# Kernel tuning notes

Measured on AMD Instinct MI355X. Metric: run time of the kernel, lower is better.

Reference implementation:

```python
import jax, jax.numpy as jnp
import numpy as np

B_TRUE, S, HEADS, DIM_HEAD, DIM, N = 2, 2, 8, 64, 512, 1024
BS = B_TRUE * S            # effective batch = (b s)
DIM_INNER = HEADS * DIM_HEAD
ALL_HEADS = S * HEADS
EPS = 1e-5


def setup_inputs() -> dict:
    key = jax.random.key(0)
    ks = jax.random.split(key, 8)
    inv = 0.02
    x = jax.random.normal(ks[0], (BS, N, DIM), dtype=jnp.float32)
    mask = jax.random.randint(ks[1], (BS, N), 0, 2).astype(bool)
    gamma = jnp.ones((DIM,), dtype=jnp.float32)
    w_qkv = jax.random.normal(ks[2], (3 * DIM_INNER, DIM), dtype=jnp.float32) * inv
    w_gates = jax.random.normal(ks[3], (HEADS, DIM), dtype=jnp.float32) * inv
    b_gates = jnp.zeros((HEADS,), dtype=jnp.float32)
    w_pre = jax.random.normal(ks[4], (ALL_HEADS, ALL_HEADS), dtype=jnp.float32) * 0.25
    w_post = jax.random.normal(ks[5], (ALL_HEADS, ALL_HEADS), dtype=jnp.float32) * 0.25
    w_out = jax.random.normal(ks[6], (DIM, DIM_INNER), dtype=jnp.float32) * inv
    return {"x": x, "mask": mask, "gamma": gamma, "w_qkv": w_qkv,
            "w_gates": w_gates, "b_gates": b_gates, "w_pre": w_pre,
            "w_post": w_post, "w_out": w_out}


def _rmsnorm(x, gamma):
    # einn.Norm('b... [d]', mean=False, bias=False): RMSNorm over last dim
    var = jnp.mean(jnp.square(x), axis=-1, keepdims=True)
    return x * jax.lax.rsqrt(var + EPS) * gamma


def reference(x, mask, gamma, w_qkv, w_gates, b_gates, w_pre, w_post, w_out):
    bs, n, dim = x.shape
    b = bs // S
    x = _rmsnorm(x, gamma)

    # QKV: 'b n (qkv h d) -> qkv b h n d'
    qkv = jnp.einsum('bnd,ed->bne', x, w_qkv)
    qkv = qkv.reshape(bs, n, 3, HEADS, DIM_HEAD).transpose(2, 0, 3, 1, 4)
    q, k, v = qkv[0], qkv[1], qkv[2]
    q = q * (DIM_HEAD ** 0.5)  # NOTE: source MULTIPLIES by sqrt(dim_head)

    sim = jnp.einsum('bhid,bhjd->bhij', q, k)  # [bs, h, n, n]
    mask_value = -jnp.finfo(sim.dtype).max

    # pre talking-heads: 1x1 conv across (s h) channels
    sim = sim.reshape(b, ALL_HEADS, n, n)
    sim = jnp.einsum('oi,binm->bonm', w_pre, sim).reshape(bs, HEADS, n, n)

    # padding mask over keys j
    sim = jnp.where(mask[:, None, None, :], sim, mask_value)

    # causal mask
    causal = jnp.triu(jnp.ones((n, n), dtype=bool), 1)
    sim = jnp.where(causal, mask_value, sim)

    attn = jax.nn.softmax(sim, axis=-1)
    post_softmax_attn = attn

    # post talking-heads
    attn = attn.reshape(b, ALL_HEADS, n, n)
    attn = jnp.einsum('oi,binm->bonm', w_post, attn).reshape(bs, HEADS, n, n)

    out = jnp.einsum('bhij,bhjd->bhid', attn, v)  # [bs, h, n, d]

    # sigmoid gates from normed x: 'b n h -> b h n 1'
    gates = jax.nn.sigmoid(jnp.einsum('bnd,hd->bnh', x, w_gates) + b_gates)
    out = out * gates.transpose(0, 2, 1)[..., None]

    # 'b h n d -> b n (h d)' then Linear(dim_inner, dim, bias=False)
    out = out.transpose(0, 2, 1, 3).reshape(bs, n, DIM_INNER)
    out = jnp.einsum('bne,de->bnd', out, w_out)
    return (out, post_softmax_attn)
```

## Files before the change

kernel.cpp:

```cpp
#include <hip/hip_runtime.h>
#include <cfloat>
#include <math.h>

#define B2   2
#define BS4  4
#define NH   8
#define DH   64
#define DIM  512
#define NSEQ 1024
#define AH   16

typedef __attribute__((ext_vector_type(8))) short short8;
typedef __attribute__((ext_vector_type(4))) float floatx4;
typedef __attribute__((ext_vector_type(2))) float float2v;

__device__ inline unsigned short f2bf(float x) {
    unsigned int u = __float_as_uint(x);
    unsigned int r = (u + 0x7fffu + ((u >> 16) & 1u)) >> 16;
    return (unsigned short)r;
}
__device__ inline float bf2f(unsigned short h) {
    return __uint_as_float(((unsigned int)h) << 16);
}
__device__ inline void split2(float x, unsigned short& h, unsigned short& l) {
    h = f2bf(x);
    l = f2bf(x - bf2f(h));
}
__device__ inline int il_addr(int k) { return ((k >> 3) << 4) + (k & 7); }

__device__ inline float2v pk_fma(float2v a, float2v b, float2v c) {
#if __has_builtin(__builtin_elementwise_fma)
    return __builtin_elementwise_fma(a, b, c);
#else
    float2v r;
    r[0] = fmaf(a[0], b[0], c[0]);
    r[1] = fmaf(a[1], b[1], c[1]);
    return r;
#endif
}

template<int MT, int NT_, bool SPLIT, bool IL>
__device__ inline void mfma_nt_core(
    const unsigned short* __restrict__ Ah, const unsigned short* __restrict__ Al,
    const unsigned short* __restrict__ Bh, const unsigned short* __restrict__ Bl,
    int K, int lda, int ldb, int arow, int bcol, floatx4 acc[MT][NT_])
{
    int lane = threadIdx.x & 63;
    int lr = lane & 15, lq = lane >> 4;
    for (int k0 = 0; k0 < K; k0 += 32) {
        const int ka = IL ? (k0 + lq * 8) * 2 : (k0 + lq * 8);
        short8 ah[MT], al[MT], bh[NT_], bl[NT_];
        #pragma unroll
        for (int mi = 0; mi < MT; ++mi) {
            size_t off = (size_t)(arow + mi * 16 + lr) * lda + ka;
            ah[mi] = *(const short8*)(Ah + off);
            if (SPLIT) al[mi] = *(const short8*)(Al + off);
        }
        #pragma unroll
        for (int ni = 0; ni < NT_; ++ni) {
            size_t off = (size_t)(bcol + ni * 16 + lr) * ldb + ka;
            bh[ni] = *(const short8*)(Bh + off);
            if (SPLIT) bl[ni] = *(const short8*)(Bl + off);
        }
        #pragma unroll
        for (int mi = 0; mi < MT; ++mi)
            #pragma unroll
            for (int ni = 0; ni < NT_; ++ni) {
                acc[mi][ni] = __builtin_amdgcn_mfma_f32_16x16x32_bf16(ah[mi], bh[ni], acc[mi][ni], 0, 0, 0);
                if (SPLIT) {
                    acc[mi][ni] = __builtin_amdgcn_mfma_f32_16x16x32_bf16(ah[mi], bl[ni], acc[mi][ni], 0, 0, 0);
                    acc[mi][ni] = __builtin_amdgcn_mfma_f32_16x16x32_bf16(al[mi], bh[ni], acc[mi][ni], 0, 0, 0);
                }
            }
    }
}

__global__ __launch_bounds__(256) void k_rmsnorm_gates(
    const float* __restrict__ x, const float* __restrict__ gamma,
    const float* __restrict__ wg, const float* __restrict__ bg,
    unsigned short* __restrict__ xn_il, float* __restrict__ gates)
{
    int r = blockIdx.x;
    int tid = threadIdx.x;
    const float* xr = x + (size_t)r * DIM;
    float v0 = xr[tid];
    float v1 = xr[tid + 256];
    float ss = v0 * v0 + v1 * v1;
    #pragma unroll
    for (int off = 32; off > 0; off >>= 1) ss += __shfl_down(ss, off, 64);
    __shared__ float sc[4];
    __shared__ float scw[NH][4];
    if ((tid & 63) == 0) sc[tid >> 6] = ss;
    __syncthreads();
    float tot = sc[0] + sc[1] + sc[2] + sc[3];
    float rs = rsqrtf(tot * (1.0f / DIM) + 1e-5f);
    float n0 = v0 * rs * gamma[tid];
    float n1 = v1 * rs * gamma[tid + 256];
    size_t rb = (size_t)r * (2 * DIM);
    unsigned short hh, ll;
    split2(n0, hh, ll);
    int a0 = il_addr(tid);
    xn_il[rb + a0] = hh; xn_il[rb + a0 + 8] = ll;
    split2(n1, hh, ll);
    int a1 = il_addr(tid + 256);
    xn_il[rb + a1] = hh; xn_il[rb + a1 + 8] = ll;
    #pragma unroll
    for (int h = 0; h < NH; ++h) {
        float p = n0 * wg[h * DIM + tid] + n1 * wg[h * DIM + tid + 256];
        #pragma unroll
        for (int off = 32; off > 0; off >>= 1) p += __shfl_down(p, off, 64);
        if ((tid & 63) == 0) scw[h][tid >> 6] = p;
    }
    __syncthreads();
    if (tid < NH) {
        float g = scw[tid][0] + scw[tid][1] + scw[tid][2] + scw[tid][3] + bg[tid];
        gates[(size_t)r * NH + tid] = 1.0f / (1.0f + __expf(-g));
    }
}

#define NQKV (3 * DIM * NH * DH)
#define NOUT (DIM * NH * DH)
__global__ __launch_bounds__(256) void k_cvt(
    const float* __restrict__ wqkv, const float* __restrict__ wout,
    unsigned short* __restrict__ wq_il, unsigned short* __restrict__ wout_b)
{
    for (int i = blockIdx.x * 256 + threadIdx.x; i < NQKV + NOUT; i += gridDim.x * 256) {
        if (i < NQKV) {
            unsigned short hh, ll;
            split2(wqkv[i], hh, ll);
            int e = i >> 9, k = i & 511;
            size_t a = (size_t)e * (2 * DIM) + il_addr(k);
            wq_il[a] = hh; wq_il[a + 8] = ll;
        } else {
            wout_b[i - NQKV] = f2bf(wout[i - NQKV]);
        }
    }
}

__global__ __launch_bounds__(64) void k_qkv_mfma(
    const unsigned short* __restrict__ xn_il, const unsigned short* __restrict__ wq_il,
    unsigned short* __restrict__ q_il, unsigned short* __restrict__ k_il,
    unsigned short* __restrict__ vT_b)
{
    __shared__ unsigned short vs[64][68];
    int bx = blockIdx.x;
    int am = blockIdx.y * 64;
    int bn = bx * 64;
    floatx4 acc[4][4];
    #pragma unroll
    for (int mi = 0; mi < 4; ++mi)
        #pragma unroll
        for (int ni = 0; ni < 4; ++ni) acc[mi][ni] = (floatx4){0.f, 0.f, 0.f, 0.f};
    mfma_nt_core<4, 4, true, true>(xn_il, xn_il + 8, wq_il, wq_il + 8,
                                   DIM, 2 * DIM, 2 * DIM, am, bn, acc);
    int tid = threadIdx.x;
    int lane = tid & 63, lr = lane & 15, lq = lane >> 4;

    if (bx < 16) {
        const bool isq = (bx < 8);
        unsigned short* dst = isq ? q_il : k_il;
        const float scale = isq ? 8.0f : 1.0f;
        #pragma unroll
        for (int mi = 0; mi < 4; ++mi)
            #pragma unroll
            for (int ni = 0; ni < 4; ++ni)
                #pragma unroll
                for (int r = 0; r < 4; ++r) {
                    int row = am + mi * 16 + lq * 4 + r;
                    int col = bn + ni * 16 + lr;
                    int bs = row >> 10, npos = row & 1023;
                    int h = (col >> 6) & 7, d = col & 63;
                    size_t base = (((size_t)(bs * 8 + h)) * NSEQ + npos) * (2 * DH) + il_addr(d);
                    unsigned short hh, ll;
                    split2(acc[mi][ni][r] * scale, hh, ll);
                    dst[base] = hh; dst[base + 8] = ll;
                }
    } else {
        const int h = bx - 16;
        const int bs = (blockIdx.y * 64) >> 10;
        const int bh = bs * 8 + h;
        const int npos_base = (blockIdx.y * 64) & 1023;
        #pragma unroll
        for (int mi = 0; mi < 4; ++mi)
            #pragma unroll
            for (int ni = 0; ni < 4; ++ni)
                #pragma unroll
                for (int r = 0; r < 4; ++r) {
                    int nl  = mi * 16 + lq * 4 + r;
                    int dl2 = ni * 16 + lr;
                    vs[dl2][nl] = f2bf(acc[mi][ni][r]);
                }
        __syncthreads();
        #pragma unroll
        for (int it = 0; it < 8; ++it) {
            int d = it * 8 + (tid >> 3);
            int c8 = (tid & 7) * 8;
            unsigned short* dst = vT_b + ((size_t)bh * DH + d) * NSEQ + npos_base + c8;
            *(ulonglong2*)dst = *(ulonglong2*)&vs[d][c8];
        }
    }
}

__global__ __launch_bounds__(64) void k_qk_mfma(
    const unsigned short* __restrict__ q_il, const unsigned short* __restrict__ k_il,
    float* __restrict__ sim_ws)
{
    __shared__ float cs[64][68];
    int am0 = blockIdx.y * 64;
    int bn0 = blockIdx.x * 64;
    if (bn0 > am0 + 63) return;
    int bh = blockIdx.z;
    int b_true = bh >> 4;
    int c = ((bh >> 3) & 1) * 8 + (bh & 7);
    const unsigned short* A = q_il + (size_t)bh * NSEQ * (2 * DH);
    const unsigned short* B = k_il + (size_t)bh * NSEQ * (2 * DH);
    floatx4 acc[4][4];
    #pragma unroll
    for (int mi = 0; mi < 4; ++mi)
        #pragma unroll
        for (int ni = 0; ni < 4; ++ni) acc[mi][ni] = (floatx4){0.f, 0.f, 0.f, 0.f};
    mfma_nt_core<4, 4, true, true>(A, A + 8, B, B + 8, DH, 2 * DH, 2 * DH, am0, bn0, acc);

    int tid = threadIdx.x;
    int lane = tid & 63, lr = lane & 15, lq = lane >> 4;
    #pragma unroll
    for (int mi = 0; mi < 4; ++mi)
        #pragma unroll
        for (int ni = 0; ni < 4; ++ni)
            #pragma unroll
            for (int r = 0; r < 4; ++r) {
                int lrow = mi * 16 + lq * 4 + r;
                int lcol = ni * 16 + lr;
                cs[lrow][lcol] = acc[mi][ni][r];
            }
    __syncthreads();
    int trow = tid >> 4;
    int tcol = (tid & 15) * 4;
    #pragma unroll
    for (int it = 0; it < 16; ++it) {
        int row = it * 4 + trow;
        float4 v4 = *(float4*)&cs[row][tcol];
        size_t gaddr = ((size_t)(b_true * NSEQ + am0 + row) * 16 + c) * NSEQ + bn0 + tcol;
        *(float4*)(sim_ws + gaddr) = v4;
    }
}

__global__ __launch_bounds__(256) void k_talk(
    float* __restrict__ sim_ws, const int* __restrict__ mask,
    const float* __restrict__ wpre, const float* __restrict__ wpost,
    float* __restrict__ probs_out)
{
    const int i = blockIdx.x;
    const int b = blockIdx.y;
    const int tid = threadIdx.x;
    const int wid = tid >> 6, lane = tid & 63;
    const int j0 = tid << 2;
    const size_t cstride = (size_t)NSEQ * NSEQ;
    float* simrow = sim_ws + (size_t)(b * NSEQ + i) * (16 * NSEQ);

    const int4 mi0 = *(const int4*)(mask + (size_t)(b * 2 + 0) * NSEQ + j0);
    const int4 mi1 = *(const int4*)(mask + (size_t)(b * 2 + 1) * NSEQ + j0);
    bool mb[2][4];
    mb[0][0] = (mi0.x != 0) && (j0 + 0 <= i);
    mb[0][1] = (mi0.y != 0) && (j0 + 1 <= i);
    mb[0][2] = (mi0.z != 0) && (j0 + 2 <= i);
    mb[0][3] = (mi0.w != 0) && (j0 + 3 <= i);
    mb[1][0] = (mi1.x != 0) && (j0 + 0 <= i);
    mb[1][1] = (mi1.y != 0) && (j0 + 1 <= i);
    mb[1][2] = (mi1.z != 0) && (j0 + 2 <= i);
    mb[1][3] = (mi1.w != 0) && (j0 + 3 <= i);

    float2v val[16][2];
    #pragma unroll
    for (int o = 0; o < 16; ++o) {
        val[o][0] = (float2v){0.f, 0.f};
        val[o][1] = (float2v){0.f, 0.f};
    }
    #pragma unroll
    for (int c = 0; c < 16; ++c) {
        float4 r = *(const float4*)(simrow + c * NSEQ + j0);
        float2v r01 = (float2v){r.x, r.y};
        float2v r23 = (float2v){r.z, r.w};
        #pragma unroll
        for (int o = 0; o < 16; ++o) {
            float w = wpre[o * 16 + c];
            float2v wv = (float2v){w, w};
            val[o][0] = pk_fma(wv, r01, val[o][0]);
            val[o][1] = pk_fma(wv, r23, val[o][1]);
        }
    }
    #pragma unroll
    for (int o = 0; o < 16; ++o) {
        const int s = o >> 3;
        if (!mb[s][0]) val[o][0][0] = -FLT_MAX;
        if (!mb[s][1]) val[o][0][1] = -FLT_MAX;
        if (!mb[s][2]) val[o][1][0] = -FLT_MAX;
        if (!mb[s][3]) val[o][1][1] = -FLT_MAX;
    }

    __shared__ float red[16][4];
    __shared__ float finmx[16];
    __shared__ float fininv[16];

    #pragma unroll
    for (int o = 0; o < 16; ++o) {
        float m = fmaxf(fmaxf(val[o][0][0], val[o][0][1]), fmaxf(val[o][1][0], val[o][1][1]));
        #pragma unroll
        for (int off = 32; off > 0; off >>= 1) m = fmaxf(m, __shfl_xor(m, off, 64));
        if (lane == 0) red[o][wid] = m;
    }
    __syncthreads();
    if (tid < 16)
        finmx[tid] = fmaxf(fmaxf(red[tid][0], red[tid][1]), fmaxf(red[tid][2], red[tid][3]));
    __syncthreads();

    #pragma unroll
    for (int o = 0; o < 16; ++o) {
        float mx = finmx[o];
        float e0 = __expf(val[o][0][0] - mx);
        float e1 = __expf(val[o][0][1] - mx);
        float e2 = __expf(val[o][1][0] - mx);
        float e3 = __expf(val[o][1][1] - mx);
        val[o][0][0] = e0; val[o][0][1] = e1;
        val[o][1][0] = e2; val[o][1][1] = e3;
        float s = (e0 + e1) + (e2 + e3);
        #pragma unroll
        for (int off = 32; off > 0; off >>= 1) s += __shfl_xor(s, off, 64);
        if (lane == 0) red[o][wid] = s;
    }
    __syncthreads();
    if (tid < 16)
        fininv[tid] = 1.0f / (red[tid][0] + red[tid][1] + red[tid][2] + red[tid][3]);
    __syncthreads();

    #pragma unroll
    for (int o = 0; o < 16; ++o) {
        float inv = fininv[o];
        float2v invv = (float2v){inv, inv};
        val[o][0] *= invv;
        val[o][1] *= invv;
        floatx4 st = {val[o][0][0], val[o][0][1], val[o][1][0], val[o][1][1]};
        __builtin_nontemporal_store(st,
            (floatx4*)(probs_out + (size_t)(b * 16 + o) * cstride + (size_t)i * NSEQ + j0));
    }

    unsigned short* a2row = (unsigned short*)simrow;
    #pragma unroll
    for (int o = 0; o < 16; ++o) {
        float2v a01 = (float2v){0.f, 0.f};
        float2v a23 = (float2v){0.f, 0.f};
        #pragma unroll
        for (int c = 0; c < 16; ++c) {
            float w = wpost[o * 16 + c];
            float2v wv = (float2v){w, w};
            a01 = pk_fma(wv, val[c][0], a01);
            a23 = pk_fma(wv, val[c][1], a23);
        }
        unsigned long long pk = (unsigned long long)f2bf(a01[0])
                              | ((unsigned long long)f2bf(a01[1]) << 16)
                              | ((unsigned long long)f2bf(a23[0]) << 32)
                              | ((unsigned long long)f2bf(a23[1]) << 48);
        *(unsigned long long*)(a2row + o * NSEQ + j0) = pk;
    }
}

__global__ __launch_bounds__(64) void k_av_mfma(
    const unsigned short* __restrict__ attn2_il, const unsigned short* __restrict__ vT_b,
    const float* __restrict__ gates, unsigned short* __restrict__ gated_b)
{
    int bh = blockIdx.y;
    int bs = bh >> 3, h = bh & 7;
    int b_true = bh >> 4;
    int c = ((bh >> 3) & 1) * 8 + (bh & 7);
    int am = blockIdx.x * 64;
    const unsigned short* Ah = attn2_il + (size_t)b_true * NSEQ * 32768 + (size_t)c * NSEQ;
    const unsigned short* Bh = vT_b + (size_t)bh * DH * NSEQ;
    floatx4 acc[4][4];
    #pragma unroll
    for (int mi = 0; mi < 4; ++mi)
        #pragma unroll
        for (int ni = 0; ni < 4; ++ni) acc[mi][ni] = (floatx4){0.f, 0.f, 0.f, 0.f};
    mfma_nt_core<4, 4, false, false>(Ah, nullptr, Bh, nullptr, NSEQ, 32768, NSEQ, am, 0, acc);
    int lane = threadIdx.x & 63, lr = lane & 15, lq = lane >> 4;
    #pragma unroll
    for (int mi = 0; mi < 4; ++mi)
        #pragma unroll
        for (int ni = 0; ni < 4; ++ni)
            #pragma unroll
            for (int r = 0; r < 4; ++r) {
                int i = am + mi * 16 + lq * 4 + r;
                int d = ni * 16 + lr;
                float g = gates[((size_t)bs * NSEQ + i) * NH + h];
                gated_b[((size_t)bs * NSEQ + i) * DIM + h * DH + d] = f2bf(acc[mi][ni][r] * g);
            }
}

__global__ __launch_bounds__(64) void k_out_mfma(
    const unsigned short* __restrict__ gated_b, const unsigned short* __restrict__ wout_b,
    float* __restrict__ out)
{
    int am = blockIdx.y * 64;
    int bn = blockIdx.x * 64;
    floatx4 acc[4][4];
    #pragma unroll
    for (int mi = 0; mi < 4; ++mi)
        #pragma unroll
        for (int ni = 0; ni < 4; ++ni) acc[mi][ni] = (floatx4){0.f, 0.f, 0.f, 0.f};
    mfma_nt_core<4, 4, false, false>(gated_b, nullptr, wout_b, nullptr, DIM, DIM, DIM, am, bn, acc);
    int lane = threadIdx.x & 63, lr = lane & 15, lq = lane >> 4;
    #pragma unroll
    for (int mi = 0; mi < 4; ++mi)
        #pragma unroll
        for (int ni = 0; ni < 4; ++ni)
            #pragma unroll
            for (int r = 0; r < 4; ++r) {
                int row = am + mi * 16 + lq * 4 + r;
                int col = bn + ni * 16 + lr;
                out[(size_t)row * DIM + col] = acc[mi][ni][r];
            }
}

extern "C" void kernel_launch(void* const* d_in, const int* in_sizes, int n_in,
                              void* d_out, int out_size, void* d_ws, size_t ws_size,
                              hipStream_t stream)
{
    (void)in_sizes; (void)n_in; (void)out_size; (void)ws_size;

    const float* x     = (const float*)d_in[0];
    const int*   mask  = (const int*)  d_in[1];
    const float* gamma = (const float*)d_in[2];
    const float* wqkv  = (const float*)d_in[3];
    const float* wg    = (const float*)d_in[4];
    const float* bg    = (const float*)d_in[5];
    const float* wpre  = (const float*)d_in[6];
    const float* wpost = (const float*)d_in[7];
    const float* wout  = (const float*)d_in[8];

    float* out       = (float*)d_out;
    float* probs_out = out + (size_t)BS4 * NSEQ * DIM;

    char* ws = (char*)d_ws;
    unsigned short* xn_il   = (unsigned short*)(ws);
    unsigned short* wq_il   = (unsigned short*)(ws + 8388608);
    unsigned short* wout_b  = (unsigned short*)(ws + 11534336);
    float*          gates   = (float*)         (ws + 12058624);
    unsigned short* q_il    = (unsigned short*)(ws + 12189696);
    unsigned short* k_il    = (unsigned short*)(ws + 20578304);
    unsigned short* vT_b    = (unsigned short*)(ws + 28966912);
    unsigned short* gated_b = (unsigned short*)(ws + 33161216);
    float*          sim_ws  = (float*)         (ws + 37355520);

    k_rmsnorm_gates<<<dim3(BS4 * NSEQ), dim3(256), 0, stream>>>(x, gamma, wg, bg, xn_il, gates);
    k_cvt<<<dim3(1024), dim3(256), 0, stream>>>(wqkv, wout, wq_il, wout_b);
    k_qkv_mfma<<<dim3(24, 64), dim3(64), 0, stream>>>(xn_il, wq_il, q_il, k_il, vT_b);
    k_qk_mfma<<<dim3(16, 16, 32), dim3(64), 0, stream>>>(q_il, k_il, sim_ws);
    k_talk<<<dim3(NSEQ, B2), dim3(256), 0, stream>>>(sim_ws, mask, wpre, wpost, probs_out);
    k_av_mfma<<<dim3(16, 32), dim3(64), 0, stream>>>((unsigned short*)sim_ws, vT_b, gates, gated_b);
    k_out_mfma<<<dim3(8, 64), dim3(64), 0, stream>>>(gated_b, wout_b, out);
}
```

Measured before the change: 373.2 us.

## Fuse prep kernels, trim softmax barriers, split-K across two waves in AV/out GEMMs

Merges the RMSNorm/gates kernel and the weight-conversion kernel into one launch, using extra blocks for the conversion. In the talking-heads softmax, each thread now reduces the per-wave partials itself, which removes two barriers and two shared-memory stages. The AV and output-projection GEMMs use two waves per block, each taking half of K, with the partials combined through shared memory. This raises parallelism in the low-occupancy GEMMs at the cost of extra LDS traffic and a barrier.

```diff
diff --git a/kernel.cpp b/kernel.cpp
--- a/kernel.cpp
+++ b/kernel.cpp
@@ -75,13 +75,34 @@
     }
 }
 
-__global__ __launch_bounds__(256) void k_rmsnorm_gates(
+#define NQKV (3 * DIM * NH * DH)
+#define NOUT (DIM * NH * DH)
+__global__ __launch_bounds__(256) void k_prep(
     const float* __restrict__ x, const float* __restrict__ gamma,
     const float* __restrict__ wg, const float* __restrict__ bg,
-    unsigned short* __restrict__ xn_il, float* __restrict__ gates)
-{
+    const float* __restrict__ wqkv, const float* __restrict__ wout,
+    unsigned short* __restrict__ xn_il, float* __restrict__ gates,
+    unsigned short* __restrict__ wq_il, unsigned short* __restrict__ wout_b)
+{
+    int tid = threadIdx.x;
+    if (blockIdx.x >= BS4 * NSEQ) {
+        int base = (blockIdx.x - BS4 * NSEQ) * 2048;
+        #pragma unroll
+        for (int e = 0; e < 8; ++e) {
+            int i = base + e * 256 + tid;
+            if (i < NQKV) {
+                unsigned short hh, ll;
+                split2(wqkv[i], hh, ll);
+                int row = i >> 9, k = i & 511;
+                size_t a = (size_t)row * (2 * DIM) + il_addr(k);
+                wq_il[a] = hh; wq_il[a + 8] = ll;
+            } else {
+                wout_b[i - NQKV] = f2bf(wout[i - NQKV]);
+            }
+        }
+        return;
+    }
     int r = blockIdx.x;
-    int tid = threadIdx.x;
     const float* xr = x + (size_t)r * DIM;
     float v0 = xr[tid];
     float v1 = xr[tid + 256];
@@ -115,25 +136,6 @@
     if (tid < NH) {
         float g = scw[tid][0] + scw[tid][1] + scw[tid][2] + scw[tid][3] + bg[tid];
         gates[(size_t)r * NH + tid] = 1.0f / (1.0f + __expf(-g));
-    }
-}
-
-#define NQKV (3 * DIM * NH * DH)
-#define NOUT (DIM * NH * DH)
-__global__ __launch_bounds__(256) void k_cvt(
-    const float* __restrict__ wqkv, const float* __restrict__ wout,
-    unsigned short* __restrict__ wq_il, unsigned short* __restrict__ wout_b)
-{
-    for (int i = blockIdx.x * 256 + threadIdx.x; i < NQKV + NOUT; i += gridDim.x * 256) {
-        if (i < NQKV) {
-            unsigned short hh, ll;
-            split2(wqkv[i], hh, ll);
-            int e = i >> 9, k = i & 511;
-            size_t a = (size_t)e * (2 * DIM) + il_addr(k);
-            wq_il[a] = hh; wq_il[a + 8] = ll;
-        } else {
-            wout_b[i - NQKV] = f2bf(wout[i - NQKV]);
-        }
     }
 }
 
@@ -298,25 +300,21 @@
         if (!mb[s][3]) val[o][1][1] = -FLT_MAX;
     }
 
-    __shared__ float red[16][4];
-    __shared__ float finmx[16];
-    __shared__ float fininv[16];
+    __shared__ float red_m[16][4];
+    __shared__ float red_s[16][4];
 
     #pragma unroll
     for (int o = 0; o < 16; ++o) {
         float m = fmaxf(fmaxf(val[o][0][0], val[o][0][1]), fmaxf(val[o][1][0], val[o][1][1]));
         #pragma unroll
         for (int off = 32; off > 0; off >>= 1) m = fmaxf(m, __shfl_xor(m, off, 64));
-        if (lane == 0) red[o][wid] = m;
-    }
-    __syncthreads();
-    if (tid < 16)
-        finmx[tid] = fmaxf(fmaxf(red[tid][0], red[tid][1]), fmaxf(red[tid][2], red[tid][3]));
-    __syncthreads();
-
-    #pragma unroll
-    for (int o = 0; o < 16; ++o) {
-        float mx = finmx[o];
+        if (lane == 0) red_m[o][wid] = m;
+    }
+    __syncthreads();
+
+    #pragma unroll
+    for (int o = 0; o < 16; ++o) {
+        float mx = fmaxf(fmaxf(red_m[o][0], red_m[o][1]), fmaxf(red_m[o][2], red_m[o][3]));
         float e0 = __expf(val[o][0][0] - mx);
         float e1 = __expf(val[o][0][1] - mx);
         float e2 = __expf(val[o][1][0] - mx);
@@ -326,16 +324,13 @@
         float s = (e0 + e1) + (e2 + e3);
         #pragma unroll
         for (int off = 32; off > 0; off >>= 1) s += __shfl_xor(s, off, 64);
-        if (lane == 0) red[o][wid] = s;
-    }
-    __syncthreads();
-    if (tid < 16)
-        fininv[tid] = 1.0f / (red[tid][0] + red[tid][1] + red[tid][2] + red[tid][3]);
-    __syncthreads();
-
-    #pragma unroll
-    for (int o = 0; o < 16; ++o) {
-        float inv = fininv[o];
+        if (lane == 0) red_s[o][wid] = s;
+    }
+    __syncthreads();
+
+    #pragma unroll
+    for (int o = 0; o < 16; ++o) {
+        float inv = 1.0f / ((red_s[o][0] + red_s[o][1]) + (red_s[o][2] + red_s[o][3]));
         float2v invv = (float2v){inv, inv};
         val[o][0] *= invv;
         val[o][1] *= invv;
@@ -364,60 +359,91 @@
     }
 }
 
-__global__ __launch_bounds__(64) void k_av_mfma(
+__global__ __launch_bounds__(128) void k_av_mfma(
     const unsigned short* __restrict__ attn2_il, const unsigned short* __restrict__ vT_b,
     const float* __restrict__ gates, unsigned short* __restrict__ gated_b)
 {
+    __shared__ float cls[64][68];
     int bh = blockIdx.y;
     int bs = bh >> 3, h = bh & 7;
     int b_true = bh >> 4;
     int c = ((bh >> 3) & 1) * 8 + (bh & 7);
     int am = blockIdx.x * 64;
-    const unsigned short* Ah = attn2_il + (size_t)b_true * NSEQ * 32768 + (size_t)c * NSEQ;
-    const unsigned short* Bh = vT_b + (size_t)bh * DH * NSEQ;
+    int w = threadIdx.x >> 6;
+    const unsigned short* Ah = attn2_il + (size_t)b_true * NSEQ * 32768 + (size_t)c * NSEQ + w * 512;
+    const unsigned short* Bh = vT_b + (size_t)bh * DH * NSEQ + w * 512;
     floatx4 acc[4][4];
     #pragma unroll
     for (int mi = 0; mi < 4; ++mi)
         #pragma unroll
         for (int ni = 0; ni < 4; ++ni) acc[mi][ni] = (floatx4){0.f, 0.f, 0.f, 0.f};
-    mfma_nt_core<4, 4, false, false>(Ah, nullptr, Bh, nullptr, NSEQ, 32768, NSEQ, am, 0, acc);
+    mfma_nt_core<4, 4, false, false>(Ah, nullptr, Bh, nullptr, 512, 32768, NSEQ, am, 0, acc);
     int lane = threadIdx.x & 63, lr = lane & 15, lq = lane >> 4;
-    #pragma unroll
-    for (int mi = 0; mi < 4; ++mi)
-        #pragma unroll
-        for (int ni = 0; ni < 4; ++ni)
-            #pragma unroll
-            for (int r = 0; r < 4; ++r) {
-                int i = am + mi * 16 + lq * 4 + r;
-                int d = ni * 16 + lr;
-                float g = gates[((size_t)bs * NSEQ + i) * NH + h];
-                gated_b[((size_t)bs * NSEQ + i) * DIM + h * DH + d] = f2bf(acc[mi][ni][r] * g);
-            }
-}
-
-__global__ __launch_bounds__(64) void k_out_mfma(
+    if (w == 1) {
+        #pragma unroll
+        for (int mi = 0; mi < 4; ++mi)
+            #pragma unroll
+            for (int ni = 0; ni < 4; ++ni)
+                #pragma unroll
+                for (int r = 0; r < 4; ++r)
+                    cls[mi * 16 + lq * 4 + r][ni * 16 + lr] = acc[mi][ni][r];
+    }
+    __syncthreads();
+    if (w == 0) {
+        #pragma unroll
+        for (int mi = 0; mi < 4; ++mi)
+            #pragma unroll
+            for (int ni = 0; ni < 4; ++ni)
+                #pragma unroll
+                for (int r = 0; r < 4; ++r) {
+                    int i = am + mi * 16 + lq * 4 + r;
+                    int d = ni * 16 + lr;
+                    float v = acc[mi][ni][r] + cls[mi * 16 + lq * 4 + r][ni * 16 + lr];
+                    float g = gates[((size_t)bs * NSEQ + i) * NH + h];
+                    gated_b[((size_t)bs * NSEQ + i) * DIM + h * DH + d] = f2bf(v * g);
+                }
+    }
+}
+
+__global__ __launch_bounds__(128) void k_out_mfma(
     const unsigned short* __restrict__ gated_b, const unsigned short* __restrict__ wout_b,
     float* __restrict__ out)
 {
+    __shared__ float cls[64][68];
     int am = blockIdx.y * 64;
     int bn = blockIdx.x * 64;
+    int w = threadIdx.x >> 6;
     floatx4 acc[4][4];
     #pragma unroll
     for (int mi = 0; mi < 4; ++mi)
         #pragma unroll
         for (int ni = 0; ni < 4; ++ni) acc[mi][ni] = (floatx4){0.f, 0.f, 0.f, 0.f};
-    mfma_nt_core<4, 4, false, false>(gated_b, nullptr, wout_b, nullptr, DIM, DIM, DIM, am, bn, acc);
+    mfma_nt_core<4, 4, false, false>(gated_b + w * 256, nullptr, wout_b + w * 256, nullptr,
+                                     256, DIM, DIM, am, bn, acc);
     int lane = threadIdx.x & 63, lr = lane & 15, lq = lane >> 4;
-    #pragma unroll
-    for (int mi = 0; mi < 4; ++mi)
-        #pragma unroll
-        for (int ni = 0; ni < 4; ++ni)
-            #pragma unroll
-            for (int r = 0; r < 4; ++r) {
-                int row = am + mi * 16 + lq * 4 + r;
-                int col = bn + ni * 16 + lr;
-                out[(size_t)row * DIM + col] = acc[mi][ni][r];
-            }
+    if (w == 1) {
+        #pragma unroll
+        for (int mi = 0; mi < 4; ++mi)
+            #pragma unroll
+            for (int ni = 0; ni < 4; ++ni)
+                #pragma unroll
+                for (int r = 0; r < 4; ++r)
+                    cls[mi * 16 + lq * 4 + r][ni * 16 + lr] = acc[mi][ni][r];
+    }
+    __syncthreads();
+    if (w == 0) {
+        #pragma unroll
+        for (int mi = 0; mi < 4; ++mi)
+            #pragma unroll
+            for (int ni = 0; ni < 4; ++ni)
+                #pragma unroll
+                for (int r = 0; r < 4; ++r) {
+                    int row = am + mi * 16 + lq * 4 + r;
+                    int col = bn + ni * 16 + lr;
+                    out[(size_t)row * DIM + col] =
+                        acc[mi][ni][r] + cls[mi * 16 + lq * 4 + r][ni * 16 + lr];
+                }
+    }
 }
 
 extern "C" void kernel_launch(void* const* d_in, const int* in_sizes, int n_in,
@@ -450,11 +476,11 @@
     unsigned short* gated_b = (unsigned short*)(ws + 33161216);
     float*          sim_ws  = (float*)         (ws + 37355520);
 
-    k_rmsnorm_gates<<<dim3(BS4 * NSEQ), dim3(256), 0, stream>>>(x, gamma, wg, bg, xn_il, gates);
-    k_cvt<<<dim3(1024), dim3(256), 0, stream>>>(wqkv, wout, wq_il, wout_b);
+    k_prep<<<dim3(BS4 * NSEQ + 512), dim3(256), 0, stream>>>(
+        x, gamma, wg, bg, wqkv, wout, xn_il, gates, wq_il, wout_b);
     k_qkv_mfma<<<dim3(24, 64), dim3(64), 0, stream>>>(xn_il, wq_il, q_il, k_il, vT_b);
     k_qk_mfma<<<dim3(16, 16, 32), dim3(64), 0, stream>>>(q_il, k_il, sim_ws);
     k_talk<<<dim3(NSEQ, B2), dim3(256), 0, stream>>>(sim_ws, mask, wpre, wpost, probs_out);
-    k_av_mfma<<<dim3(16, 32), dim3(64), 0, stream>>>((unsigned short*)sim_ws, vT_b, gates, gated_b);
-    k_out_mfma<<<dim3(8, 64), dim3(64), 0, stream>>>(gated_b, wout_b, out);
-}
+    k_av_mfma<<<dim3(16, 32), dim3(128), 0, stream>>>((unsigned short*)sim_ws, vT_b, gates, gated_b);
+    k_out_mfma<<<dim3(8, 64), dim3(128), 0, stream>>>(gated_b, wout_b, out);
+}
```

Result: no change. 366.0 us, median of 2 (-1.9%).
